# Kernel optimization log

Measured on AMD Instinct MI355X. Metric: run time of the kernel, lower is better.

Reference implementation:

```python
import jax, jax.numpy as jnp
import numpy as np

B, L, D, H = 2, 2048, 1024, 16
C = D // H  # head dim = 64
SCALE = 1.0 / np.sqrt(D).astype(np.float32)  # note: 1/sqrt(in_c), full dim, per source


def setup_inputs() -> dict:
    key = jax.random.key(0)
    ks = jax.random.split(key, 5)
    return {
        "x": jax.random.normal(ks[0], (B, L, D), dtype=jnp.float32),
        "w_qkv": jax.random.normal(ks[1], (3 * D, D), dtype=jnp.float32) * (1.0 / np.sqrt(D)),
        "b_qkv": jax.random.normal(ks[2], (3 * D,), dtype=jnp.float32) * 0.02,
        "w_o": jax.random.normal(ks[3], (D, D), dtype=jnp.float32) * (1.0 / np.sqrt(D)),
        "b_o": jax.random.normal(ks[4], (D,), dtype=jnp.float32) * 0.02,
    }


def reference(x, w_qkv, b_qkv, w_o, b_o):
    b, l, d = x.shape
    h, c = H, d // H
    # fused QKV projection: torch Linear is x @ W.T + b
    qkv = jnp.einsum('bld,ed->ble', x, w_qkv) + b_qkv  # [B, L, 3D]
    q, k, v = jnp.split(qkv, 3, axis=-1)
    q = q.reshape(b, l, h, c)
    k = k.reshape(b, l, h, c)
    v = v.reshape(b, l, h, c)
    # attention scores [B, H, L, L], scaled by 1/sqrt(in_c)
    attn = jax.nn.softmax(jnp.einsum('blhc,bmhc->bhlm', q, k) * SCALE, axis=-1)
    heads = jnp.einsum('bhlm,bmhc->blhc', attn, v).reshape(b, l, d)
    return jnp.einsum('bld,ed->ble', heads, w_o) + b_o + x
```

## Files before the change

kernel.cpp:

```cpp
#include <hip/hip_runtime.h>
#include <hip/hip_bf16.h>
#include <stdint.h>

typedef _Float16 half_t;
typedef _Float16 half4 __attribute__((ext_vector_type(4)));
typedef _Float16 half8 __attribute__((ext_vector_type(8)));
typedef float f32x4 __attribute__((ext_vector_type(4)));

#define SCALE2_ 0.045084220f

#if __has_builtin(__builtin_amdgcn_exp2f)
#define EXP2F(x) __builtin_amdgcn_exp2f(x)
#else
#define EXP2F(x) exp2f(x)
#endif

#define GLL16(g, l)                                                        \
  __builtin_amdgcn_global_load_lds(                                        \
      (const __attribute__((address_space(1))) void*)(g),                  \
      (__attribute__((address_space(3))) void*)(l), 16, 0, 0)

__global__ void cvt_all(const float* __restrict__ x,
                        const float* __restrict__ wqkv,
                        const float* __restrict__ wo,
                        half_t* __restrict__ xb,
                        half_t* __restrict__ wqkvb,
                        half_t* __restrict__ wob) {
  int i = blockIdx.x * blockDim.x + threadIdx.x;
  const float* src; half_t* dst; int off;
  if (i < 1048576)       { src = x;    dst = xb;    off = i; }
  else if (i < 1835008)  { src = wqkv; dst = wqkvb; off = i - 1048576; }
  else                   { src = wo;   dst = wob;   off = i - 1835008; }
  float4 v = ((const float4*)src)[off];
  half4 h;
  h[0] = (half_t)v.x; h[1] = (half_t)v.y; h[2] = (half_t)v.z; h[3] = (half_t)v.w;
  ((half4*)dst)[off] = h;
}

__global__ __launch_bounds__(256) void qkv_gemm(
    const half_t* __restrict__ A, const half_t* __restrict__ Bw,
    const float* __restrict__ bias,
    half_t* __restrict__ Qh, half_t* __restrict__ Kh, half_t* __restrict__ Vt) {
  __shared__ __align__(16) half_t As[128 * 32];
  __shared__ __align__(16) half_t Bs[128 * 32];
  const int tid = threadIdx.x;
  const int wave = tid >> 6, lane = tid & 63;
  const int t = lane & 15, g = lane >> 4;
  const int wr = (wave >> 1) * 64, wc = (wave & 1) * 64;
  const int m0 = blockIdx.y * 128, n0 = blockIdx.x * 128;

  f32x4 acc[4][4];
#pragma unroll
  for (int i = 0; i < 4; ++i)
#pragma unroll
    for (int j = 0; j < 4; ++j) acc[i][j] = (f32x4){0.f, 0.f, 0.f, 0.f};

  const int srow = tid >> 2, schunk = (tid & 3) * 8;
  const half_t* aptr = A + (size_t)(m0 + srow) * 1024 + schunk;
  const half_t* bptr = Bw + (size_t)(n0 + srow) * 1024 + schunk;
  char* asb = (char*)As + wave * 1024;
  char* bsb = (char*)Bs + wave * 1024;

  for (int kk = 0; kk < 1024; kk += 32) {
    GLL16(aptr, asb);
    GLL16(aptr + 64 * 1024, asb + 4096);
    GLL16(bptr, bsb);
    GLL16(bptr + 64 * 1024, bsb + 4096);
    aptr += 32; bptr += 32;
    __syncthreads();

    half8 af[4], bf[4];
#pragma unroll
    for (int fm = 0; fm < 4; ++fm)
      af[fm] = *(const half8*)&As[(wr + fm * 16 + t) * 32 + g * 8];
#pragma unroll
    for (int fn = 0; fn < 4; ++fn)
      bf[fn] = *(const half8*)&Bs[(wc + fn * 16 + t) * 32 + g * 8];
#pragma unroll
    for (int fm = 0; fm < 4; ++fm)
#pragma unroll
      for (int fn = 0; fn < 4; ++fn)
        acc[fm][fn] = __builtin_amdgcn_mfma_f32_16x16x32_f16(
            af[fm], bf[fn], acc[fm][fn], 0, 0, 0);
    __syncthreads();
  }

#pragma unroll
  for (int fm = 0; fm < 4; ++fm) {
    const int mb = m0 + wr + fm * 16 + g * 4;
#pragma unroll
    for (int fn = 0; fn < 4; ++fn) {
      const int n = n0 + wc + fn * 16 + t;
      const float bv = bias[n];
      const int sec = n >> 10, nn = n & 1023;
      const int h = nn >> 6, c = nn & 63;
#pragma unroll
      for (int r = 0; r < 4; ++r) {
        const int mm = mb + r;
        const int b = mm >> 11, l = mm & 2047;
        const float v = acc[fm][fn][r] + bv;
        const size_t bh = (size_t)(b * 16 + h);
        if (sec == 0)      Qh[(bh * 2048 + l) * 64 + c] = (half_t)(v * SCALE2_);
        else if (sec == 1) Kh[(bh * 2048 + l) * 64 + c] = (half_t)v;
        else {
          const int lp = (l & ~63) |
                         (((l >> 2) & 3) * 16 + ((l >> 4) & 3) * 4 + (l & 3));
          Vt[(bh * 64 + c) * 2048 + lp] = (half_t)v;
        }
      }
    }
  }
}

__global__ __launch_bounds__(256) void attn_kernel(
    const half_t* __restrict__ Qh, const half_t* __restrict__ Kh,
    const half_t* __restrict__ Vt, half_t* __restrict__ Hd) {
  __shared__ __align__(16) char lds_raw[2][2][8192];
  const int bh = blockIdx.x;
  const int qt = blockIdx.y;
  const int tid = threadIdx.x;
  const int wave = tid >> 6, lane = tid & 63;
  const int t = lane & 15, g = lane >> 4;

  const half_t* Q = Qh + ((size_t)bh * 2048 + qt * 64 + wave * 16) * 64;
  const half_t* Kbase = Kh + (size_t)bh * 2048 * 64;
  const half_t* Vbase = Vt + (size_t)bh * 64 * 2048;

  const half8 q0 = *(const half8*)&Q[t * 64 + g * 8];
  const half8 q1 = *(const half8*)&Q[t * 64 + 32 + g * 8];

  const int swz = (t & 7) << 4;
  const int vk0 = t * 128 + ((g * 16) ^ swz);
  const int vk1 = t * 128 + ((64 + g * 16) ^ swz);
  const int vv0 = t * 128 + ((g * 32) ^ swz);
  const int vv1 = t * 128 + ((g * 32 + 16) ^ swz);

  f32x4 o[4];
#pragma unroll
  for (int i = 0; i < 4; ++i) o[i] = (f32x4){0.f, 0.f, 0.f, 0.f};
  float m_run = -1e30f, l_run = 0.f;

#define STAGE_TILE(bufi, mt_)                                                 \
  {                                                                           \
    char* kb_ = lds_raw[bufi][0];                                             \
    char* vb_ = lds_raw[bufi][1];                                             \
    _Pragma("unroll")                                                         \
    for (int is = 0; is < 2; ++is) {                                          \
      const int s = tid + is * 256;                                           \
      const int r = s >> 3, rb = (s & 7) * 16;                                \
      const int cb = rb ^ ((r & 7) << 4);                                     \
      GLL16(Kbase + (size_t)((mt_) + r) * 64 + (cb >> 1),                     \
            kb_ + (wave * 64 + is * 256) * 16);                               \
      GLL16(Vbase + (size_t)r * 2048 + (mt_) + (cb >> 1),                     \
            vb_ + (wave * 64 + is * 256) * 16);                               \
    }                                                                         \
  }

  STAGE_TILE(0, 0);
  __syncthreads();

  for (int it = 0; it < 32; ++it) {
    const int mt = it * 64;
    const int cur = it & 1;
    if (it + 1 < 32) STAGE_TILE(cur ^ 1, mt + 64);

    const char* kb = lds_raw[cur][0];
    const char* vb = lds_raw[cur][1];

    f32x4 s4[4];
    __builtin_amdgcn_s_setprio(1);
#pragma unroll
    for (int st = 0; st < 4; ++st) {
      half8 k0 = *(const half8*)(kb + vk0 + st * 2048);
      half8 k1 = *(const half8*)(kb + vk1 + st * 2048);
      f32x4 a = (f32x4){0.f, 0.f, 0.f, 0.f};
      a = __builtin_amdgcn_mfma_f32_16x16x32_f16(k0, q0, a, 0, 0, 0);
      a = __builtin_amdgcn_mfma_f32_16x16x32_f16(k1, q1, a, 0, 0, 0);
      s4[st] = a;
    }
    __builtin_amdgcn_s_setprio(0);

    float tm = fmaxf(fmaxf(fmaxf(s4[0][0], s4[0][1]), fmaxf(s4[0][2], s4[0][3])),
                     fmaxf(fmaxf(s4[1][0], s4[1][1]), fmaxf(s4[1][2], s4[1][3])));
    tm = fmaxf(tm,
         fmaxf(fmaxf(fmaxf(s4[2][0], s4[2][1]), fmaxf(s4[2][2], s4[2][3])),
               fmaxf(fmaxf(s4[3][0], s4[3][1]), fmaxf(s4[3][2], s4[3][3]))));
    tm = fmaxf(tm, __shfl_xor(tm, 16));
    tm = fmaxf(tm, __shfl_xor(tm, 32));

    if (!__all(tm <= m_run + 10.f)) {
      const float mnew = fmaxf(m_run, tm);
      const float corr = EXP2F(m_run - mnew);
      m_run = mnew;
      l_run *= corr;
#pragma unroll
      for (int r = 0; r < 4; ++r) {
        const float cv = __shfl(corr, (g << 2) + r);
#pragma unroll
        for (int ct = 0; ct < 4; ++ct) o[ct][r] *= cv;
      }
    }

    float rs = 0.f;
    half4 pf[4];
#pragma unroll
    for (int st = 0; st < 4; ++st) {
      const float p0 = EXP2F(s4[st][0] - m_run);
      const float p1 = EXP2F(s4[st][1] - m_run);
      const float p2 = EXP2F(s4[st][2] - m_run);
      const float p3 = EXP2F(s4[st][3] - m_run);
      rs += (p0 + p1) + (p2 + p3);
      pf[st][0] = (half_t)p0; pf[st][1] = (half_t)p1;
      pf[st][2] = (half_t)p2; pf[st][3] = (half_t)p3;
    }
    rs += __shfl_xor(rs, 16);
    rs += __shfl_xor(rs, 32);
    l_run += rs;

    __builtin_amdgcn_s_setprio(1);
#pragma unroll
    for (int sthalf = 0; sthalf < 2; ++sthalf) {
      const int voff = sthalf ? vv1 : vv0;
#pragma unroll
      for (int ct = 0; ct < 4; ++ct) {
        half8 vv = *(const half8*)(vb + voff + ct * 2048);
        half4 vlo = {vv[0], vv[1], vv[2], vv[3]};
        half4 vhi = {vv[4], vv[5], vv[6], vv[7]};
        o[ct] = __builtin_amdgcn_mfma_f32_16x16x16f16(pf[2 * sthalf], vlo,
                                                      o[ct], 0, 0, 0);
        o[ct] = __builtin_amdgcn_mfma_f32_16x16x16f16(pf[2 * sthalf + 1], vhi,
                                                      o[ct], 0, 0, 0);
      }
    }
    __builtin_amdgcn_s_setprio(0);

    __syncthreads();
  }

  const int b = bh >> 4, h = bh & 15;
#pragma unroll
  for (int r = 0; r < 4; ++r) {
    const float li = 1.f / __shfl(l_run, (g << 2) + r);
    const size_t row = (size_t)b * 2048 + qt * 64 + wave * 16 + g * 4 + r;
#pragma unroll
    for (int ct = 0; ct < 4; ++ct)
      Hd[row * 1024 + h * 64 + ct * 16 + t] = (half_t)(o[ct][r] * li);
  }
#undef STAGE_TILE
}

__global__ __launch_bounds__(256) void out_gemm(
    const half_t* __restrict__ A, const half_t* __restrict__ Bw,
    const float* __restrict__ bias, const float* __restrict__ xres,
    float* __restrict__ out) {
  __shared__ __align__(16) half_t As[128 * 32];
  __shared__ __align__(16) half_t Bs[128 * 32];
  const int tid = threadIdx.x;
  const int wave = tid >> 6, lane = tid & 63;
  const int t = lane & 15, g = lane >> 4;
  const int wr = (wave >> 1) * 64, wc = (wave & 1) * 64;
  const int m0 = blockIdx.y * 128, n0 = blockIdx.x * 128;

  f32x4 acc[4][4];
#pragma unroll
  for (int i = 0; i < 4; ++i)
#pragma unroll
    for (int j = 0; j < 4; ++j) acc[i][j] = (f32x4){0.f, 0.f, 0.f, 0.f};

  const int srow = tid >> 2, schunk = (tid & 3) * 8;
  const half_t* aptr = A + (size_t)(m0 + srow) * 1024 + schunk;
  const half_t* bptr = Bw + (size_t)(n0 + srow) * 1024 + schunk;
  char* asb = (char*)As + wave * 1024;
  char* bsb = (char*)Bs + wave * 1024;

  for (int kk = 0; kk < 1024; kk += 32) {
    GLL16(aptr, asb);
    GLL16(aptr + 64 * 1024, asb + 4096);
    GLL16(bptr, bsb);
    GLL16(bptr + 64 * 1024, bsb + 4096);
    aptr += 32; bptr += 32;
    __syncthreads();

    half8 af[4], bf[4];
#pragma unroll
    for (int fm = 0; fm < 4; ++fm)
      af[fm] = *(const half8*)&As[(wr + fm * 16 + t) * 32 + g * 8];
#pragma unroll
    for (int fn = 0; fn < 4; ++fn)
      bf[fn] = *(const half8*)&Bs[(wc + fn * 16 + t) * 32 + g * 8];
#pragma unroll
    for (int fm = 0; fm < 4; ++fm)
#pragma unroll
      for (int fn = 0; fn < 4; ++fn)
        acc[fm][fn] = __builtin_amdgcn_mfma_f32_16x16x32_f16(
            af[fm], bf[fn], acc[fm][fn], 0, 0, 0);
    __syncthreads();
  }

#pragma unroll
  for (int fm = 0; fm < 4; ++fm) {
    const int mb = m0 + wr + fm * 16 + g * 4;
#pragma unroll
    for (int fn = 0; fn < 4; ++fn) {
      const int n = n0 + wc + fn * 16 + t;
      const float bv = bias[n];
#pragma unroll
      for (int r = 0; r < 4; ++r) {
        const size_t idx = (size_t)(mb + r) * 1024 + n;
        out[idx] = acc[fm][fn][r] + bv + xres[idx];
      }
    }
  }
}

extern "C" void kernel_launch(void* const* d_in, const int* in_sizes, int n_in,
                              void* d_out, int out_size, void* d_ws, size_t ws_size,
                              hipStream_t stream) {
  const float* x     = (const float*)d_in[0];
  const float* w_qkv = (const float*)d_in[1];
  const float* b_qkv = (const float*)d_in[2];
  const float* w_o   = (const float*)d_in[3];
  const float* b_o   = (const float*)d_in[4];
  float* out = (float*)d_out;

  char* ws = (char*)d_ws;
  half_t* xb    = (half_t*)(ws + 0);
  half_t* wqkvb = (half_t*)(ws + (size_t)8  * 1048576);
  half_t* wob   = (half_t*)(ws + (size_t)14 * 1048576);
  half_t* Qh    = (half_t*)(ws + (size_t)16 * 1048576);
  half_t* Kh    = (half_t*)(ws + (size_t)24 * 1048576);
  half_t* Vt    = (half_t*)(ws + (size_t)32 * 1048576);
  half_t* Hd    = (half_t*)(ws + (size_t)40 * 1048576);

  cvt_all<<<8192, 256, 0, stream>>>(x, w_qkv, w_o, xb, wqkvb, wob);
  qkv_gemm<<<dim3(24, 32), 256, 0, stream>>>(xb, wqkvb, b_qkv, Qh, Kh, Vt);
  attn_kernel<<<dim3(32, 32), 256, 0, stream>>>(Qh, Kh, Vt, Hd);
  out_gemm<<<dim3(8, 32), 256, 0, stream>>>(Hd, wob, b_o, x, out);
}
```

Before: 218.9 us.

## Deepen GEMM K-tiles with swizzled LDS, widen attention blocks, shrink out_gemm tile

The QKV and output GEMMs now stage 64-wide K slices, with an XOR swizzle on the LDS layout to avoid bank conflicts, which halves the number of barrier iterations. The out_gemm M tile drops to 64 so the grid doubles to 512 blocks for better CU occupancy. Attention blocks grow to 512 threads covering 128 query rows, so each staged K/V tile is shared by 8 waves with one load per thread. The row-max reduction in the softmax is also regrouped. Larger LDS tiles and bigger blocks may lower occupancy.

```diff
diff --git a/kernel.cpp b/kernel.cpp
--- a/kernel.cpp
+++ b/kernel.cpp
@@ -41,8 +41,8 @@
     const half_t* __restrict__ A, const half_t* __restrict__ Bw,
     const float* __restrict__ bias,
     half_t* __restrict__ Qh, half_t* __restrict__ Kh, half_t* __restrict__ Vt) {
-  __shared__ __align__(16) half_t As[128 * 32];
-  __shared__ __align__(16) half_t Bs[128 * 32];
+  __shared__ __align__(16) half_t As[128 * 64];
+  __shared__ __align__(16) half_t Bs[128 * 64];
   const int tid = threadIdx.x;
   const int wave = tid >> 6, lane = tid & 63;
   const int t = lane & 15, g = lane >> 4;
@@ -55,33 +55,39 @@
 #pragma unroll
     for (int j = 0; j < 4; ++j) acc[i][j] = (f32x4){0.f, 0.f, 0.f, 0.f};
 
-  const int srow = tid >> 2, schunk = (tid & 3) * 8;
-  const half_t* aptr = A + (size_t)(m0 + srow) * 1024 + schunk;
-  const half_t* bptr = Bw + (size_t)(n0 + srow) * 1024 + schunk;
-  char* asb = (char*)As + wave * 1024;
-  char* bsb = (char*)Bs + wave * 1024;
-
-  for (int kk = 0; kk < 1024; kk += 32) {
-    GLL16(aptr, asb);
-    GLL16(aptr + 64 * 1024, asb + 4096);
-    GLL16(bptr, bsb);
-    GLL16(bptr + 64 * 1024, bsb + 4096);
-    aptr += 32; bptr += 32;
-    __syncthreads();
-
-    half8 af[4], bf[4];
-#pragma unroll
-    for (int fm = 0; fm < 4; ++fm)
-      af[fm] = *(const half8*)&As[(wr + fm * 16 + t) * 32 + g * 8];
-#pragma unroll
-    for (int fn = 0; fn < 4; ++fn)
-      bf[fn] = *(const half8*)&Bs[(wc + fn * 16 + t) * 32 + g * 8];
-#pragma unroll
-    for (int fm = 0; fm < 4; ++fm)
+  const int r0 = tid >> 3;
+  const int colb = ((tid & 7) * 16) ^ ((r0 & 7) << 4);
+  const half_t* aptr = A + (size_t)(m0 + r0) * 1024 + (colb >> 1);
+  const half_t* bptr = Bw + (size_t)(n0 + r0) * 1024 + (colb >> 1);
+  const int swz = (t & 7) << 4;
+
+  for (int kk = 0; kk < 16; ++kk) {
+#pragma unroll
+    for (int is = 0; is < 4; ++is) {
+      GLL16(aptr + (size_t)is * 32 * 1024, (char*)As + wave * 1024 + is * 4096);
+      GLL16(bptr + (size_t)is * 32 * 1024, (char*)Bs + wave * 1024 + is * 4096);
+    }
+    aptr += 64; bptr += 64;
+    __syncthreads();
+
+#pragma unroll
+    for (int h = 0; h < 2; ++h) {
+      half8 af[4], bf[4];
+#pragma unroll
+      for (int fm = 0; fm < 4; ++fm)
+        af[fm] = *(const half8*)((const char*)As + (wr + fm * 16 + t) * 128 +
+                                 ((h * 64 + g * 16) ^ swz));
 #pragma unroll
       for (int fn = 0; fn < 4; ++fn)
-        acc[fm][fn] = __builtin_amdgcn_mfma_f32_16x16x32_f16(
-            af[fm], bf[fn], acc[fm][fn], 0, 0, 0);
+        bf[fn] = *(const half8*)((const char*)Bs + (wc + fn * 16 + t) * 128 +
+                                 ((h * 64 + g * 16) ^ swz));
+#pragma unroll
+      for (int fm = 0; fm < 4; ++fm)
+#pragma unroll
+        for (int fn = 0; fn < 4; ++fn)
+          acc[fm][fn] = __builtin_amdgcn_mfma_f32_16x16x32_f16(
+              af[fm], bf[fn], acc[fm][fn], 0, 0, 0);
+    }
     __syncthreads();
   }
 
@@ -112,7 +118,7 @@
   }
 }
 
-__global__ __launch_bounds__(256) void attn_kernel(
+__global__ __launch_bounds__(512) void attn_kernel(
     const half_t* __restrict__ Qh, const half_t* __restrict__ Kh,
     const half_t* __restrict__ Vt, half_t* __restrict__ Hd) {
   __shared__ __align__(16) char lds_raw[2][2][8192];
@@ -122,12 +128,14 @@
   const int wave = tid >> 6, lane = tid & 63;
   const int t = lane & 15, g = lane >> 4;
 
-  const half_t* Q = Qh + ((size_t)bh * 2048 + qt * 64 + wave * 16) * 64;
-  const half_t* Kbase = Kh + (size_t)bh * 2048 * 64;
-  const half_t* Vbase = Vt + (size_t)bh * 64 * 2048;
-
+  const half_t* Q = Qh + ((size_t)bh * 2048 + qt * 128 + wave * 16) * 64;
   const half8 q0 = *(const half8*)&Q[t * 64 + g * 8];
   const half8 q1 = *(const half8*)&Q[t * 64 + 32 + g * 8];
+
+  const int r0 = tid >> 3;
+  const int colb = ((tid & 7) * 16) ^ ((r0 & 7) << 4);
+  const half_t* kptr = Kh + (size_t)bh * 2048 * 64 + (size_t)r0 * 64 + (colb >> 1);
+  const half_t* vptr = Vt + (size_t)bh * 64 * 2048 + (size_t)r0 * 2048 + (colb >> 1);
 
   const int swz = (t & 7) << 4;
   const int vk0 = t * 128 + ((g * 16) ^ swz);
@@ -140,29 +148,19 @@
   for (int i = 0; i < 4; ++i) o[i] = (f32x4){0.f, 0.f, 0.f, 0.f};
   float m_run = -1e30f, l_run = 0.f;
 
-#define STAGE_TILE(bufi, mt_)                                                 \
-  {                                                                           \
-    char* kb_ = lds_raw[bufi][0];                                             \
-    char* vb_ = lds_raw[bufi][1];                                             \
-    _Pragma("unroll")                                                         \
-    for (int is = 0; is < 2; ++is) {                                          \
-      const int s = tid + is * 256;                                           \
-      const int r = s >> 3, rb = (s & 7) * 16;                                \
-      const int cb = rb ^ ((r & 7) << 4);                                     \
-      GLL16(Kbase + (size_t)((mt_) + r) * 64 + (cb >> 1),                     \
-            kb_ + (wave * 64 + is * 256) * 16);                               \
-      GLL16(Vbase + (size_t)r * 2048 + (mt_) + (cb >> 1),                     \
-            vb_ + (wave * 64 + is * 256) * 16);                               \
-    }                                                                         \
-  }
-
-  STAGE_TILE(0, 0);
+#define STG(bufi)                                                \
+  {                                                              \
+    GLL16(kptr, (char*)lds_raw[bufi][0] + wave * 1024);          \
+    GLL16(vptr, (char*)lds_raw[bufi][1] + wave * 1024);          \
+    kptr += 4096; vptr += 64;                                    \
+  }
+
+  STG(0);
   __syncthreads();
 
   for (int it = 0; it < 32; ++it) {
-    const int mt = it * 64;
     const int cur = it & 1;
-    if (it + 1 < 32) STAGE_TILE(cur ^ 1, mt + 64);
+    if (it + 1 < 32) STG(cur ^ 1);
 
     const char* kb = lds_raw[cur][0];
     const char* vb = lds_raw[cur][1];
@@ -180,11 +178,12 @@
     }
     __builtin_amdgcn_s_setprio(0);
 
-    float tm = fmaxf(fmaxf(fmaxf(s4[0][0], s4[0][1]), fmaxf(s4[0][2], s4[0][3])),
-                     fmaxf(fmaxf(s4[1][0], s4[1][1]), fmaxf(s4[1][2], s4[1][3])));
-    tm = fmaxf(tm,
-         fmaxf(fmaxf(fmaxf(s4[2][0], s4[2][1]), fmaxf(s4[2][2], s4[2][3])),
-               fmaxf(fmaxf(s4[3][0], s4[3][1]), fmaxf(s4[3][2], s4[3][3]))));
+    float a0 = fmaxf(fmaxf(s4[0][0], s4[0][1]), s4[0][2]);
+    float a1 = fmaxf(fmaxf(s4[0][3], s4[1][0]), s4[1][1]);
+    float a2 = fmaxf(fmaxf(s4[1][2], s4[1][3]), s4[2][0]);
+    float a3 = fmaxf(fmaxf(s4[2][1], s4[2][2]), s4[2][3]);
+    float a4 = fmaxf(fmaxf(s4[3][0], s4[3][1]), s4[3][2]);
+    float tm = fmaxf(fmaxf(fmaxf(a0, a1), a2), fmaxf(fmaxf(a3, a4), s4[3][3]));
     tm = fmaxf(tm, __shfl_xor(tm, 16));
     tm = fmaxf(tm, __shfl_xor(tm, 32));
 
@@ -241,64 +240,71 @@
 #pragma unroll
   for (int r = 0; r < 4; ++r) {
     const float li = 1.f / __shfl(l_run, (g << 2) + r);
-    const size_t row = (size_t)b * 2048 + qt * 64 + wave * 16 + g * 4 + r;
+    const size_t row = (size_t)b * 2048 + qt * 128 + wave * 16 + g * 4 + r;
 #pragma unroll
     for (int ct = 0; ct < 4; ++ct)
       Hd[row * 1024 + h * 64 + ct * 16 + t] = (half_t)(o[ct][r] * li);
   }
-#undef STAGE_TILE
+#undef STG
 }
 
 __global__ __launch_bounds__(256) void out_gemm(
     const half_t* __restrict__ A, const half_t* __restrict__ Bw,
     const float* __restrict__ bias, const float* __restrict__ xres,
     float* __restrict__ out) {
-  __shared__ __align__(16) half_t As[128 * 32];
-  __shared__ __align__(16) half_t Bs[128 * 32];
+  __shared__ __align__(16) half_t As[64 * 64];
+  __shared__ __align__(16) half_t Bs[128 * 64];
   const int tid = threadIdx.x;
   const int wave = tid >> 6, lane = tid & 63;
   const int t = lane & 15, g = lane >> 4;
-  const int wr = (wave >> 1) * 64, wc = (wave & 1) * 64;
-  const int m0 = blockIdx.y * 128, n0 = blockIdx.x * 128;
-
-  f32x4 acc[4][4];
-#pragma unroll
-  for (int i = 0; i < 4; ++i)
+  const int wr = (wave >> 1) * 32, wc = (wave & 1) * 64;
+  const int m0 = blockIdx.y * 64, n0 = blockIdx.x * 128;
+
+  f32x4 acc[2][4];
+#pragma unroll
+  for (int i = 0; i < 2; ++i)
 #pragma unroll
     for (int j = 0; j < 4; ++j) acc[i][j] = (f32x4){0.f, 0.f, 0.f, 0.f};
 
-  const int srow = tid >> 2, schunk = (tid & 3) * 8;
-  const half_t* aptr = A + (size_t)(m0 + srow) * 1024 + schunk;
-  const half_t* bptr = Bw + (size_t)(n0 + srow) * 1024 + schunk;
-  char* asb = (char*)As + wave * 1024;
-  char* bsb = (char*)Bs + wave * 1024;
-
-  for (int kk = 0; kk < 1024; kk += 32) {
-    GLL16(aptr, asb);
-    GLL16(aptr + 64 * 1024, asb + 4096);
-    GLL16(bptr, bsb);
-    GLL16(bptr + 64 * 1024, bsb + 4096);
-    aptr += 32; bptr += 32;
-    __syncthreads();
-
-    half8 af[4], bf[4];
-#pragma unroll
-    for (int fm = 0; fm < 4; ++fm)
-      af[fm] = *(const half8*)&As[(wr + fm * 16 + t) * 32 + g * 8];
-#pragma unroll
-    for (int fn = 0; fn < 4; ++fn)
-      bf[fn] = *(const half8*)&Bs[(wc + fn * 16 + t) * 32 + g * 8];
-#pragma unroll
-    for (int fm = 0; fm < 4; ++fm)
+  const int r0 = tid >> 3;
+  const int colb = ((tid & 7) * 16) ^ ((r0 & 7) << 4);
+  const half_t* aptr = A + (size_t)(m0 + r0) * 1024 + (colb >> 1);
+  const half_t* bptr = Bw + (size_t)(n0 + r0) * 1024 + (colb >> 1);
+  const int swz = (t & 7) << 4;
+
+  for (int kk = 0; kk < 16; ++kk) {
+#pragma unroll
+    for (int is = 0; is < 2; ++is)
+      GLL16(aptr + (size_t)is * 32 * 1024, (char*)As + wave * 1024 + is * 4096);
+#pragma unroll
+    for (int is = 0; is < 4; ++is)
+      GLL16(bptr + (size_t)is * 32 * 1024, (char*)Bs + wave * 1024 + is * 4096);
+    aptr += 64; bptr += 64;
+    __syncthreads();
+
+#pragma unroll
+    for (int h = 0; h < 2; ++h) {
+      half8 af[2], bf[4];
+#pragma unroll
+      for (int fm = 0; fm < 2; ++fm)
+        af[fm] = *(const half8*)((const char*)As + (wr + fm * 16 + t) * 128 +
+                                 ((h * 64 + g * 16) ^ swz));
 #pragma unroll
       for (int fn = 0; fn < 4; ++fn)
-        acc[fm][fn] = __builtin_amdgcn_mfma_f32_16x16x32_f16(
-            af[fm], bf[fn], acc[fm][fn], 0, 0, 0);
-    __syncthreads();
-  }
-
-#pragma unroll
-  for (int fm = 0; fm < 4; ++fm) {
+        bf[fn] = *(const half8*)((const char*)Bs + (wc + fn * 16 + t) * 128 +
+                                 ((h * 64 + g * 16) ^ swz));
+#pragma unroll
+      for (int fm = 0; fm < 2; ++fm)
+#pragma unroll
+        for (int fn = 0; fn < 4; ++fn)
+          acc[fm][fn] = __builtin_amdgcn_mfma_f32_16x16x32_f16(
+              af[fm], bf[fn], acc[fm][fn], 0, 0, 0);
+    }
+    __syncthreads();
+  }
+
+#pragma unroll
+  for (int fm = 0; fm < 2; ++fm) {
     const int mb = m0 + wr + fm * 16 + g * 4;
 #pragma unroll
     for (int fn = 0; fn < 4; ++fn) {
@@ -334,6 +340,6 @@
 
   cvt_all<<<8192, 256, 0, stream>>>(x, w_qkv, w_o, xb, wqkvb, wob);
   qkv_gemm<<<dim3(24, 32), 256, 0, stream>>>(xb, wqkvb, b_qkv, Qh, Kh, Vt);
-  attn_kernel<<<dim3(32, 32), 256, 0, stream>>>(Qh, Kh, Vt, Hd);
-  out_gemm<<<dim3(8, 32), 256, 0, stream>>>(Hd, wob, b_o, x, out);
-}
+  attn_kernel<<<dim3(32, 16), 512, 0, stream>>>(Qh, Kh, Vt, Hd);
+  out_gemm<<<dim3(8, 64), 256, 0, stream>>>(Hd, wob, b_o, x, out);
+}
```

New measurement: 204.4 us. -6.6%, faster.
